# Optimization experiments

Measured on AMD Instinct MI355X. Metric: run time of the kernel, lower is better.

## Reference

```python
import jax, jax.numpy as jnp
import numpy as np

IN_FEATURES = 16080
TREES = 64
LEAVES = 128
CLASSES = 16
BATCH = 64


def setup_inputs() -> dict:
    key = jax.random.key(0)
    k_x, k_w, k_b, k_c = jax.random.split(key, 4)
    x = jax.random.normal(k_x, (BATCH, TREES, IN_FEATURES), dtype=jnp.float32)
    # nn.Linear(16080, leaves): weight [leaves, in], bias [leaves]
    lim = 1.0 / np.sqrt(IN_FEATURES)
    W = jax.random.uniform(k_w, (LEAVES, IN_FEATURES), minval=-lim, maxval=lim, dtype=jnp.float32)
    b = jax.random.uniform(k_b, (LEAVES,), minval=-lim, maxval=lim, dtype=jnp.float32)
    # contribution parameter ~ U(-1, 1), shape [trees, leaves, classes]
    contribution = jax.random.uniform(k_c, (TREES, LEAVES, CLASSES), minval=-1.0, maxval=1.0, dtype=jnp.float32)
    return {"x": x, "W": W, "b": b, "contribution": contribution}


def reference(x, W, b, contribution):
    # Linear + Hardtanh: [B, T, L]
    symbolic_paths = jnp.clip(jnp.einsum('bti,li->btl', x, W) + b, -1.0, 1.0)
    # Fused form of the per-(tree,leaf) outer-product loop: [B, T, L, C]
    class_value = symbolic_paths[..., None] * contribution[None]
    p = jax.nn.softmax(class_value, axis=-1)
    # 1 - sum(p^2) over classes (Gini-style impurity): [B, T, L]
    class_value = jnp.sum(1.0 - p * p, axis=-1)
    return (symbolic_paths, class_value)
```

## Files before the change

kernel.cpp:

```cpp
#include <hip/hip_runtime.h>
#include <hip/hip_bf16.h>
#include <stdint.h>

#define IN_F   16080
#define NTREES 64
#define NLEAF  128
#define NCLS   16
#define NBATCH 64
#define M_TOT  (NBATCH*NTREES)
#define OUT_HALF (M_TOT*NLEAF)

#define BM 64
#define BN 128
#define BK 64
#define KSPLIT 16
#define NSTEPS ((IN_F + BK - 1)/BK)

typedef __attribute__((ext_vector_type(8))) short short8;
typedef __attribute__((ext_vector_type(4))) float f32x4;

typedef const __attribute__((address_space(1))) uint32_t gu32_t;
typedef __attribute__((address_space(3))) uint32_t su32_t;

__device__ __forceinline__ short8 cvt8(float4 lo, float4 hi){
  union { short8 s8; __hip_bfloat162 h2[4]; } u;
  u.h2[0] = __float22bfloat162_rn(make_float2(lo.x, lo.y));
  u.h2[1] = __float22bfloat162_rn(make_float2(lo.z, lo.w));
  u.h2[2] = __float22bfloat162_rn(make_float2(hi.x, hi.y));
  u.h2[3] = __float22bfloat162_rn(make_float2(hi.z, hi.w));
  return u.s8;
}

__global__ __launch_bounds__(256)
void wcvt_kernel(const float* __restrict__ W, short* __restrict__ Wb){
  int i = (blockIdx.x * 256 + threadIdx.x) << 3;
  float4 a = *(const float4*)(W + i);
  float4 b = *(const float4*)(W + i + 4);
  *(short8*)(Wb + i) = cvt8(a, b);
}

__global__ __launch_bounds__(256, 4)
void gemm_slab_kernel(const float* __restrict__ X,
                      const short* __restrict__ Wb,
                      float* __restrict__ accbuf,
                      const short* __restrict__ zeropage){
  __shared__ __align__(16) short BsH[2][NLEAF * BK];

  const int tid = threadIdx.x;
  const int m0  = blockIdx.x * BM;
  const int kc  = blockIdx.y;
  const int s0  = (kc * NSTEPS) / KSPLIT;
  const int s1  = ((kc + 1) * NSTEPS) / KSPLIT;

  const int lane = tid & 63;
  const int wv   = tid >> 6;
  const int wm   = wv & 1;
  const int wn   = wv >> 1;
  const int fr   = lane & 15;
  const int fq   = lane >> 4;

  f32x4 acc[2][4];
  #pragma unroll
  for (int mt = 0; mt < 2; ++mt)
    #pragma unroll
    for (int nt = 0; nt < 4; ++nt) acc[mt][nt] = (f32x4){0.f,0.f,0.f,0.f};

  float4 av[2][2][2];
  const float* arow[2];
  arow[0] = X + (size_t)(m0 + wm*32 + 0*16 + fr) * IN_F;
  arow[1] = X + (size_t)(m0 + wm*32 + 1*16 + fr) * IN_F;

  {
    const int k0 = s0 * BK;
    #pragma unroll
    for (int j = 0; j < 4; ++j){
      int lin = j*256 + tid;
      int r   = lin >> 3;
      int c   = (lin & 7) ^ (r & 7);
      int gk  = k0 + (c << 3);
      const short* gp = (gk + 8 <= IN_F) ? (Wb + (size_t)r * IN_F + gk)
                                         : zeropage;
      __builtin_amdgcn_global_load_lds((gu32_t*)gp, (su32_t*)(&BsH[0][0] + lin*8),
                                       16, 0, 0);
    }
    #pragma unroll
    for (int mt = 0; mt < 2; ++mt)
      #pragma unroll
      for (int h = 0; h < 2; ++h)
        #pragma unroll
        for (int q = 0; q < 2; ++q){
          int gk = k0 + h*32 + fq*8 + q*4;
          av[mt][h][q] = (gk + 4 <= IN_F) ? *(const float4*)(arow[mt] + gk)
                                          : make_float4(0.f,0.f,0.f,0.f);
        }
  }

  for (int s = s0; s < s1; ++s){
    const int par = (s - s0) & 1;
    short* bcur = &BsH[par][0];
    short* bnxt = &BsH[par ^ 1][0];

    {
      const int k1 = (s + 1) * BK;
      #pragma unroll
      for (int j = 0; j < 4; ++j){
        int lin = j*256 + tid;
        int r   = lin >> 3;
        int c   = (lin & 7) ^ (r & 7);
        int gk  = k1 + (c << 3);
        const short* gp = (gk + 8 <= IN_F) ? (Wb + (size_t)r * IN_F + gk)
                                           : zeropage;
        __builtin_amdgcn_global_load_lds((gu32_t*)gp, (su32_t*)(bnxt + lin*8),
                                         16, 0, 0);
      }
    }

    asm volatile("s_waitcnt vmcnt(4)" ::: "memory");
    __builtin_amdgcn_s_barrier();

    short8 af[2][2];
    #pragma unroll
    for (int mt = 0; mt < 2; ++mt)
      #pragma unroll
      for (int h = 0; h < 2; ++h)
        af[mt][h] = cvt8(av[mt][h][0], av[mt][h][1]);

    {
      const int k1 = (s + 1) * BK;
      #pragma unroll
      for (int mt = 0; mt < 2; ++mt)
        #pragma unroll
        for (int h = 0; h < 2; ++h)
          #pragma unroll
          for (int q = 0; q < 2; ++q){
            int gk = k1 + h*32 + fq*8 + q*4;
            av[mt][h][q] = (gk + 4 <= IN_F) ? *(const float4*)(arow[mt] + gk)
                                            : make_float4(0.f,0.f,0.f,0.f);
          }
    }

    #pragma unroll
    for (int nt = 0; nt < 4; ++nt){
      const int l  = wn*64 + nt*16 + fr;
      const int xw = l & 7;
      const short* rowb = bcur + l*BK;
      #pragma unroll
      for (int h = 0; h < 2; ++h){
        int cc = (((h << 2) + fq) ^ xw) << 3;
        short8 bf = *(const short8*)(rowb + cc);
        #pragma unroll
        for (int mt = 0; mt < 2; ++mt)
          acc[mt][nt] = __builtin_amdgcn_mfma_f32_16x16x32_bf16(
                            af[mt][h], bf, acc[mt][nt], 0, 0, 0);
      }
    }

    __builtin_amdgcn_s_barrier();
  }

  #pragma unroll
  for (int mt = 0; mt < 2; ++mt){
    const int rbase = m0 + wm*32 + mt*16 + fq*4;
    #pragma unroll
    for (int nt = 0; nt < 4; ++nt){
      int col = wn*64 + nt*16 + fr;
      #pragma unroll
      for (int r = 0; r < 4; ++r)
        accbuf[(size_t)kc * OUT_HALF + (size_t)(rbase + r) * NLEAF + col]
            = acc[mt][nt][r];
    }
  }
}

__global__ __launch_bounds__(256)
void epilogue_slab_kernel(const float* __restrict__ slabs,
                          float* __restrict__ out,
                          const float* __restrict__ bias,
                          const float* __restrict__ contrib){
  int idx = blockIdx.x * 256 + threadIdx.x;
  int l   = idx & (NLEAF - 1);
  int row = idx >> 7;
  int t   = row & (NTREES - 1);

  float s = 0.f;
  #pragma unroll
  for (int kc = 0; kc < KSPLIT; ++kc)
    s += slabs[(size_t)kc * OUT_HALF + idx];
  s += bias[l];
  s = fminf(1.f, fmaxf(-1.f, s));
  out[idx] = s;

  const float4* cp = (const float4*)(contrib + (((size_t)t * NLEAF + l) << 4));
  float4 c0 = cp[0], c1 = cp[1], c2 = cp[2], c3 = cp[3];
  float v[16] = { s*c0.x, s*c0.y, s*c0.z, s*c0.w,
                  s*c1.x, s*c1.y, s*c1.z, s*c1.w,
                  s*c2.x, s*c2.y, s*c2.z, s*c2.w,
                  s*c3.x, s*c3.y, s*c3.z, s*c3.w };
  float m = v[0];
  #pragma unroll
  for (int c = 1; c < 16; ++c) m = fmaxf(m, v[c]);
  float se = 0.f, se2 = 0.f;
  #pragma unroll
  for (int c = 0; c < 16; ++c){
    float e = __expf(v[c] - m);
    se  += e;
    se2 += e * e;
  }
  out[OUT_HALF + idx] = (float)NCLS - se2 / (se * se);
}

__global__ __launch_bounds__(256, 4)
void gemm_atomic_kernel(const float* __restrict__ X,
                        const float* __restrict__ Wg,
                        float* __restrict__ accbuf,
                        const float* __restrict__ zeropage){
  __shared__ __align__(16) float BsF[BN * BK];

  const int tid = threadIdx.x;
  const int m0  = blockIdx.x * BM;
  const int kc  = blockIdx.y;
  const int s0  = (kc * NSTEPS) / KSPLIT;
  const int s1  = ((kc + 1) * NSTEPS) / KSPLIT;

  const int lane = tid & 63;
  const int wv   = tid >> 6;
  const int wm   = wv & 1;
  const int wn   = wv >> 1;
  const int fr   = lane & 15;
  const int fq   = lane >> 4;

  f32x4 acc[2][4];
  #pragma unroll
  for (int mt = 0; mt < 2; ++mt)
    #pragma unroll
    for (int nt = 0; nt < 4; ++nt) acc[mt][nt] = (f32x4){0.f,0.f,0.f,0.f};

  for (int s = s0; s < s1; ++s){
    const int k0 = s * BK;
    __syncthreads();

    float4 av[2][2][2];
    #pragma unroll
    for (int mt = 0; mt < 2; ++mt){
      const float* rowp = X + (size_t)(m0 + wm*32 + mt*16 + fr) * IN_F;
      #pragma unroll
      for (int h = 0; h < 2; ++h)
        #pragma unroll
        for (int q = 0; q < 2; ++q){
          int gk = k0 + h*32 + fq*8 + q*4;
          av[mt][h][q] = (gk + 4 <= IN_F) ? *(const float4*)(rowp + gk)
                                          : make_float4(0.f,0.f,0.f,0.f);
        }
    }

    #pragma unroll
    for (int j = 0; j < 8; ++j){
      int lin = j*256 + tid;
      int r   = lin >> 4;
      int p   = lin & 15;
      int c   = p ^ (r & 7);
      int gk  = k0 + c*4;
      const float* gp = (gk + 4 <= IN_F) ? (Wg + (size_t)r * IN_F + gk)
                                         : zeropage;
      __builtin_amdgcn_global_load_lds((gu32_t*)gp, (su32_t*)(BsF + lin*4),
                                       16, 0, 0);
    }

    short8 af[2][2];
    #pragma unroll
    for (int mt = 0; mt < 2; ++mt)
      #pragma unroll
      for (int h = 0; h < 2; ++h)
        af[mt][h] = cvt8(av[mt][h][0], av[mt][h][1]);

    __syncthreads();

    #pragma unroll
    for (int nt = 0; nt < 4; ++nt){
      const int l  = wn*64 + nt*16 + fr;
      const int xw = l & 7;
      const float* rowb = BsF + l*64;
      #pragma unroll
      for (int h = 0; h < 2; ++h){
        int c0 = h*8 + fq*2;
        float4 b0 = *(const float4*)(rowb + ((c0    ) ^ xw)*4);
        float4 b1 = *(const float4*)(rowb + ((c0 + 1) ^ xw)*4);
        short8 bf = cvt8(b0, b1);
        #pragma unroll
        for (int mt = 0; mt < 2; ++mt)
          acc[mt][nt] = __builtin_amdgcn_mfma_f32_16x16x32_bf16(
                            af[mt][h], bf, acc[mt][nt], 0, 0, 0);
      }
    }
  }

  #pragma unroll
  for (int mt = 0; mt < 2; ++mt){
    const int rbase = m0 + wm*32 + mt*16 + fq*4;
    #pragma unroll
    for (int nt = 0; nt < 4; ++nt){
      int col = wn*64 + nt*16 + fr;
      #pragma unroll
      for (int r = 0; r < 4; ++r)
        atomicAdd(&accbuf[(size_t)(rbase + r) * NLEAF + col], acc[mt][nt][r]);
    }
  }
}

__global__ __launch_bounds__(256)
void epilogue_inplace_kernel(float* __restrict__ out,
                             const float* __restrict__ bias,
                             const float* __restrict__ contrib){
  int idx = blockIdx.x * 256 + threadIdx.x;
  int l   = idx & (NLEAF - 1);
  int row = idx >> 7;
  int t   = row & (NTREES - 1);

  float s = out[idx] + bias[l];
  s = fminf(1.f, fmaxf(-1.f, s));
  out[idx] = s;

  const float4* cp = (const float4*)(contrib + (((size_t)t * NLEAF + l) << 4));
  float4 c0 = cp[0], c1 = cp[1], c2 = cp[2], c3 = cp[3];
  float v[16] = { s*c0.x, s*c0.y, s*c0.z, s*c0.w,
                  s*c1.x, s*c1.y, s*c1.z, s*c1.w,
                  s*c2.x, s*c2.y, s*c2.z, s*c2.w,
                  s*c3.x, s*c3.y, s*c3.z, s*c3.w };
  float m = v[0];
  #pragma unroll
  for (int c = 1; c < 16; ++c) m = fmaxf(m, v[c]);
  float se = 0.f, se2 = 0.f;
  #pragma unroll
  for (int c = 0; c < 16; ++c){
    float e = __expf(v[c] - m);
    se  += e;
    se2 += e * e;
  }
  out[OUT_HALF + idx] = (float)NCLS - se2 / (se * se);
}

extern "C" void kernel_launch(void* const* d_in, const int* in_sizes, int n_in,
                              void* d_out, int out_size, void* d_ws, size_t ws_size,
                              hipStream_t stream){
  const float* X       = (const float*)d_in[0];
  const float* Wg      = (const float*)d_in[1];
  const float* bias    = (const float*)d_in[2];
  const float* contrib = (const float*)d_in[3];
  float* out = (float*)d_out;

  const size_t SLAB_BYTES = (size_t)KSPLIT * OUT_HALF * sizeof(float);
  const size_t WB_BYTES   = (size_t)NLEAF * IN_F * sizeof(short);
  char* ws = (char*)d_ws;
  const int WCVT_BLOCKS = (NLEAF * IN_F) / (256 * 8);

  dim3 g1(M_TOT / BM, KSPLIT);

  if (ws_size >= SLAB_BYTES + WB_BYTES + 256){
    float* slabs = (float*)ws;
    short* Wb    = (short*)(ws + SLAB_BYTES);
    short* zp    = (short*)(ws + SLAB_BYTES + WB_BYTES);
    hipMemsetAsync(zp, 0, 256, stream);
    wcvt_kernel<<<WCVT_BLOCKS, 256, 0, stream>>>(Wg, Wb);
    gemm_slab_kernel<<<g1, 256, 0, stream>>>(X, Wb, slabs, zp);
    epilogue_slab_kernel<<<OUT_HALF / 256, 256, 0, stream>>>(slabs, out, bias, contrib);
  } else {
    hipMemsetAsync(out, 0, (size_t)OUT_HALF * sizeof(float), stream);
    hipMemsetAsync(ws, 0, 256, stream);
    gemm_atomic_kernel<<<g1, 256, 0, stream>>>(X, Wg, out, (const float*)ws);
    epilogue_inplace_kernel<<<OUT_HALF / 256, 256, 0, stream>>>(out, bias, contrib);
  }
}
```

Measured before the change: 400.5 us.

## Fuse split-K reduction and epilogue into GEMM via last-block ticket counter

```diff
diff --git a/kernel.cpp b/kernel.cpp
--- a/kernel.cpp
+++ b/kernel.cpp
@@ -15,6 +15,7 @@
 #define BK 64
 #define KSPLIT 16
 #define NSTEPS ((IN_F + BK - 1)/BK)
+#define NMBLK  (M_TOT / BM)
 
 typedef __attribute__((ext_vector_type(8))) short short8;
 typedef __attribute__((ext_vector_type(4))) float f32x4;
@@ -32,7 +33,9 @@
 }
 
 __global__ __launch_bounds__(256)
-void wcvt_kernel(const float* __restrict__ W, short* __restrict__ Wb){
+void wcvt_kernel(const float* __restrict__ W, short* __restrict__ Wb,
+                 uint32_t* __restrict__ zpt){
+  if (blockIdx.x == 0 && threadIdx.x < 128) zpt[threadIdx.x] = 0u;
   int i = (blockIdx.x * 256 + threadIdx.x) << 3;
   float4 a = *(const float4*)(W + i);
   float4 b = *(const float4*)(W + i + 4);
@@ -42,12 +45,18 @@
 __global__ __launch_bounds__(256, 4)
 void gemm_slab_kernel(const float* __restrict__ X,
                       const short* __restrict__ Wb,
-                      float* __restrict__ accbuf,
-                      const short* __restrict__ zeropage){
+                      float* __restrict__ slabs,
+                      const short* __restrict__ zeropage,
+                      int* __restrict__ tickets,
+                      float* __restrict__ out,
+                      const float* __restrict__ bias,
+                      const float* __restrict__ contrib){
   __shared__ __align__(16) short BsH[2][NLEAF * BK];
+  __shared__ int s_last;
 
   const int tid = threadIdx.x;
-  const int m0  = blockIdx.x * BM;
+  const int mb  = blockIdx.x;
+  const int m0  = mb * BM;
   const int kc  = blockIdx.y;
   const int s0  = (kc * NSTEPS) / KSPLIT;
   const int s1  = ((kc + 1) * NSTEPS) / KSPLIT;
@@ -166,47 +175,54 @@
       int col = wn*64 + nt*16 + fr;
       #pragma unroll
       for (int r = 0; r < 4; ++r)
-        accbuf[(size_t)kc * OUT_HALF + (size_t)(rbase + r) * NLEAF + col]
+        slabs[(size_t)kc * OUT_HALF + (size_t)(rbase + r) * NLEAF + col]
             = acc[mt][nt][r];
     }
   }
-}
-
-__global__ __launch_bounds__(256)
-void epilogue_slab_kernel(const float* __restrict__ slabs,
-                          float* __restrict__ out,
-                          const float* __restrict__ bias,
-                          const float* __restrict__ contrib){
-  int idx = blockIdx.x * 256 + threadIdx.x;
-  int l   = idx & (NLEAF - 1);
-  int row = idx >> 7;
-  int t   = row & (NTREES - 1);
-
-  float s = 0.f;
-  #pragma unroll
-  for (int kc = 0; kc < KSPLIT; ++kc)
-    s += slabs[(size_t)kc * OUT_HALF + idx];
-  s += bias[l];
-  s = fminf(1.f, fmaxf(-1.f, s));
-  out[idx] = s;
-
-  const float4* cp = (const float4*)(contrib + (((size_t)t * NLEAF + l) << 4));
-  float4 c0 = cp[0], c1 = cp[1], c2 = cp[2], c3 = cp[3];
-  float v[16] = { s*c0.x, s*c0.y, s*c0.z, s*c0.w,
-                  s*c1.x, s*c1.y, s*c1.z, s*c1.w,
-                  s*c2.x, s*c2.y, s*c2.z, s*c2.w,
-                  s*c3.x, s*c3.y, s*c3.z, s*c3.w };
-  float m = v[0];
-  #pragma unroll
-  for (int c = 1; c < 16; ++c) m = fmaxf(m, v[c]);
-  float se = 0.f, se2 = 0.f;
-  #pragma unroll
-  for (int c = 0; c < 16; ++c){
-    float e = __expf(v[c] - m);
-    se  += e;
-    se2 += e * e;
-  }
-  out[OUT_HALF + idx] = (float)NCLS - se2 / (se * se);
+
+  __syncthreads();
+  if (tid == 0){
+    __builtin_amdgcn_fence(__ATOMIC_RELEASE, "agent");
+    int old = atomicAdd(&tickets[mb], 1);
+    s_last = (old == KSPLIT - 1) ? 1 : 0;
+  }
+  __syncthreads();
+  if (!s_last) return;
+
+  __builtin_amdgcn_fence(__ATOMIC_ACQUIRE, "agent");
+
+  const size_t obase = (size_t)m0 * NLEAF;
+  for (int j = 0; j < (BM * NLEAF) / 256; ++j){
+    const int    il  = j * 256 + tid;
+    const size_t idx = obase + il;
+    const int    l   = il & (NLEAF - 1);
+    const int    t   = (il >> 7) & (NTREES - 1);
+
+    float sum = 0.f;
+    #pragma unroll
+    for (int k = 0; k < KSPLIT; ++k)
+      sum += slabs[(size_t)k * OUT_HALF + idx];
+    float sv = fminf(1.f, fmaxf(-1.f, sum + bias[l]));
+    out[idx] = sv;
+
+    const float4* cp = (const float4*)(contrib + (((size_t)t * NLEAF + l) << 4));
+    float4 c0 = cp[0], c1 = cp[1], c2 = cp[2], c3 = cp[3];
+    float v[16] = { sv*c0.x, sv*c0.y, sv*c0.z, sv*c0.w,
+                    sv*c1.x, sv*c1.y, sv*c1.z, sv*c1.w,
+                    sv*c2.x, sv*c2.y, sv*c2.z, sv*c2.w,
+                    sv*c3.x, sv*c3.y, sv*c3.z, sv*c3.w };
+    float mx = v[0];
+    #pragma unroll
+    for (int c = 1; c < 16; ++c) mx = fmaxf(mx, v[c]);
+    float se = 0.f, se2 = 0.f;
+    #pragma unroll
+    for (int c = 0; c < 16; ++c){
+      float e = __expf(v[c] - mx);
+      se  += e;
+      se2 += e * e;
+    }
+    out[OUT_HALF + idx] = (float)NCLS - se2 / (se * se);
+  }
 }
 
 __global__ __launch_bounds__(256, 4)
@@ -353,16 +369,17 @@
   char* ws = (char*)d_ws;
   const int WCVT_BLOCKS = (NLEAF * IN_F) / (256 * 8);
 
-  dim3 g1(M_TOT / BM, KSPLIT);
-
-  if (ws_size >= SLAB_BYTES + WB_BYTES + 256){
-    float* slabs = (float*)ws;
-    short* Wb    = (short*)(ws + SLAB_BYTES);
-    short* zp    = (short*)(ws + SLAB_BYTES + WB_BYTES);
-    hipMemsetAsync(zp, 0, 256, stream);
-    wcvt_kernel<<<WCVT_BLOCKS, 256, 0, stream>>>(Wg, Wb);
-    gemm_slab_kernel<<<g1, 256, 0, stream>>>(X, Wb, slabs, zp);
-    epilogue_slab_kernel<<<OUT_HALF / 256, 256, 0, stream>>>(slabs, out, bias, contrib);
+  dim3 g1(NMBLK, KSPLIT);
+
+  if (ws_size >= SLAB_BYTES + WB_BYTES + 512){
+    float* slabs   = (float*)ws;
+    short* Wb      = (short*)(ws + SLAB_BYTES);
+    int*   tickets = (int*)(ws + SLAB_BYTES + WB_BYTES);
+    short* zp      = (short*)(ws + SLAB_BYTES + WB_BYTES + 256);
+    wcvt_kernel<<<WCVT_BLOCKS, 256, 0, stream>>>(Wg, Wb,
+                   (uint32_t*)(ws + SLAB_BYTES + WB_BYTES));
+    gemm_slab_kernel<<<g1, 256, 0, stream>>>(X, Wb, slabs, zp, tickets,
+                                             out, bias, contrib);
   } else {
     hipMemsetAsync(out, 0, (size_t)OUT_HALF * sizeof(float), stream);
     hipMemsetAsync(ws, 0, 256, stream);
```

Measured after the change: 464.8 us. 16.1% more time.

## Give each wave 16 rows by all 128 leaves; fold zero-page memset into convert kernel

Applied to the files above, without the earlier changes.

```diff
diff --git a/kernel.cpp b/kernel.cpp
--- a/kernel.cpp
+++ b/kernel.cpp
@@ -15,6 +15,7 @@
 #define BK 64
 #define KSPLIT 16
 #define NSTEPS ((IN_F + BK - 1)/BK)
+#define NMBLK  (M_TOT / BM)
 
 typedef __attribute__((ext_vector_type(8))) short short8;
 typedef __attribute__((ext_vector_type(4))) float f32x4;
@@ -32,7 +33,9 @@
 }
 
 __global__ __launch_bounds__(256)
-void wcvt_kernel(const float* __restrict__ W, short* __restrict__ Wb){
+void wcvt_kernel(const float* __restrict__ W, short* __restrict__ Wb,
+                 uint32_t* __restrict__ zp){
+  if (blockIdx.x == 0 && threadIdx.x < 64) zp[threadIdx.x] = 0u;
   int i = (blockIdx.x * 256 + threadIdx.x) << 3;
   float4 a = *(const float4*)(W + i);
   float4 b = *(const float4*)(W + i + 4);
@@ -42,7 +45,7 @@
 __global__ __launch_bounds__(256, 4)
 void gemm_slab_kernel(const float* __restrict__ X,
                       const short* __restrict__ Wb,
-                      float* __restrict__ accbuf,
+                      float* __restrict__ slabs,
                       const short* __restrict__ zeropage){
   __shared__ __align__(16) short BsH[2][NLEAF * BK];
 
@@ -54,21 +57,15 @@
 
   const int lane = tid & 63;
   const int wv   = tid >> 6;
-  const int wm   = wv & 1;
-  const int wn   = wv >> 1;
   const int fr   = lane & 15;
   const int fq   = lane >> 4;
 
-  f32x4 acc[2][4];
-  #pragma unroll
-  for (int mt = 0; mt < 2; ++mt)
-    #pragma unroll
-    for (int nt = 0; nt < 4; ++nt) acc[mt][nt] = (f32x4){0.f,0.f,0.f,0.f};
-
-  float4 av[2][2][2];
-  const float* arow[2];
-  arow[0] = X + (size_t)(m0 + wm*32 + 0*16 + fr) * IN_F;
-  arow[1] = X + (size_t)(m0 + wm*32 + 1*16 + fr) * IN_F;
+  f32x4 acc[8];
+  #pragma unroll
+  for (int nt = 0; nt < 8; ++nt) acc[nt] = (f32x4){0.f,0.f,0.f,0.f};
+
+  float4 av[2][2];
+  const float* arow = X + (size_t)(m0 + wv*16 + fr) * IN_F;
 
   {
     const int k0 = s0 * BK;
@@ -84,15 +81,13 @@
                                        16, 0, 0);
     }
     #pragma unroll
-    for (int mt = 0; mt < 2; ++mt)
-      #pragma unroll
-      for (int h = 0; h < 2; ++h)
-        #pragma unroll
-        for (int q = 0; q < 2; ++q){
-          int gk = k0 + h*32 + fq*8 + q*4;
-          av[mt][h][q] = (gk + 4 <= IN_F) ? *(const float4*)(arow[mt] + gk)
-                                          : make_float4(0.f,0.f,0.f,0.f);
-        }
+    for (int h = 0; h < 2; ++h)
+      #pragma unroll
+      for (int q = 0; q < 2; ++q){
+        int gk = k0 + h*32 + fq*8 + q*4;
+        av[h][q] = (gk + 4 <= IN_F) ? *(const float4*)(arow + gk)
+                                    : make_float4(0.f,0.f,0.f,0.f);
+      }
   }
 
   for (int s = s0; s < s1; ++s){
@@ -118,57 +113,48 @@
     asm volatile("s_waitcnt vmcnt(4)" ::: "memory");
     __builtin_amdgcn_s_barrier();
 
-    short8 af[2][2];
-    #pragma unroll
-    for (int mt = 0; mt < 2; ++mt)
-      #pragma unroll
-      for (int h = 0; h < 2; ++h)
-        af[mt][h] = cvt8(av[mt][h][0], av[mt][h][1]);
+    short8 af[2];
+    #pragma unroll
+    for (int h = 0; h < 2; ++h)
+      af[h] = cvt8(av[h][0], av[h][1]);
 
     {
       const int k1 = (s + 1) * BK;
       #pragma unroll
-      for (int mt = 0; mt < 2; ++mt)
+      for (int h = 0; h < 2; ++h)
         #pragma unroll
-        for (int h = 0; h < 2; ++h)
-          #pragma unroll
-          for (int q = 0; q < 2; ++q){
-            int gk = k1 + h*32 + fq*8 + q*4;
-            av[mt][h][q] = (gk + 4 <= IN_F) ? *(const float4*)(arow[mt] + gk)
-                                            : make_float4(0.f,0.f,0.f,0.f);
-          }
-    }
-
-    #pragma unroll
-    for (int nt = 0; nt < 4; ++nt){
-      const int l  = wn*64 + nt*16 + fr;
+        for (int q = 0; q < 2; ++q){
+          int gk = k1 + h*32 + fq*8 + q*4;
+          av[h][q] = (gk + 4 <= IN_F) ? *(const float4*)(arow + gk)
+                                      : make_float4(0.f,0.f,0.f,0.f);
+        }
+    }
+
+    #pragma unroll
+    for (int nt = 0; nt < 8; ++nt){
+      const int l  = nt*16 + fr;
       const int xw = l & 7;
       const short* rowb = bcur + l*BK;
       #pragma unroll
       for (int h = 0; h < 2; ++h){
         int cc = (((h << 2) + fq) ^ xw) << 3;
         short8 bf = *(const short8*)(rowb + cc);
-        #pragma unroll
-        for (int mt = 0; mt < 2; ++mt)
-          acc[mt][nt] = __builtin_amdgcn_mfma_f32_16x16x32_bf16(
-                            af[mt][h], bf, acc[mt][nt], 0, 0, 0);
+        acc[nt] = __builtin_amdgcn_mfma_f32_16x16x32_bf16(
+                      af[h], bf, acc[nt], 0, 0, 0);
       }
     }
 
     __builtin_amdgcn_s_barrier();
   }
 
-  #pragma unroll
-  for (int mt = 0; mt < 2; ++mt){
-    const int rbase = m0 + wm*32 + mt*16 + fq*4;
-    #pragma unroll
-    for (int nt = 0; nt < 4; ++nt){
-      int col = wn*64 + nt*16 + fr;
-      #pragma unroll
-      for (int r = 0; r < 4; ++r)
-        accbuf[(size_t)kc * OUT_HALF + (size_t)(rbase + r) * NLEAF + col]
-            = acc[mt][nt][r];
-    }
+  const int rbase = m0 + wv*16 + fq*4;
+  #pragma unroll
+  for (int nt = 0; nt < 8; ++nt){
+    int col = nt*16 + fr;
+    #pragma unroll
+    for (int r = 0; r < 4; ++r)
+      slabs[(size_t)kc * OUT_HALF + (size_t)(rbase + r) * NLEAF + col]
+          = acc[nt][r];
   }
 }
 
@@ -353,14 +339,13 @@
   char* ws = (char*)d_ws;
   const int WCVT_BLOCKS = (NLEAF * IN_F) / (256 * 8);
 
-  dim3 g1(M_TOT / BM, KSPLIT);
+  dim3 g1(NMBLK, KSPLIT);
 
   if (ws_size >= SLAB_BYTES + WB_BYTES + 256){
     float* slabs = (float*)ws;
     short* Wb    = (short*)(ws + SLAB_BYTES);
     short* zp    = (short*)(ws + SLAB_BYTES + WB_BYTES);
-    hipMemsetAsync(zp, 0, 256, stream);
-    wcvt_kernel<<<WCVT_BLOCKS, 256, 0, stream>>>(Wg, Wb);
+    wcvt_kernel<<<WCVT_BLOCKS, 256, 0, stream>>>(Wg, Wb, (uint32_t*)zp);
     gemm_slab_kernel<<<g1, 256, 0, stream>>>(X, Wb, slabs, zp);
     epilogue_slab_kernel<<<OUT_HALF / 256, 256, 0, stream>>>(slabs, out, bias, contrib);
   } else {
```

Result: no change. 393.5 us (-1.7%).
